# Optimization experiments

Hardware: AMD Instinct MI355X
Metric: run time of the kernel (lower is better)

The kernel has to match this reference:

```python
import jax, jax.numpy as jnp
import numpy as np

N_HEAD = 16
N_KV_HEADS = 4
N_REP = 4
HEAD_DIM = 128
N_EMBD = 2048
EPS = 1e-5
ROPE_BASE = 10000.0


def setup_inputs() -> dict:
    key = jax.random.key(0)
    ks = jax.random.split(key, 5)
    B, T, C = 2, 2048, N_EMBD
    s = 0.02
    return {
        "x": jax.random.normal(ks[0], (B, T, C), dtype=jnp.float32),
        "wq": jax.random.normal(ks[1], (C, N_HEAD * HEAD_DIM), dtype=jnp.float32) * s,
        "wk": jax.random.normal(ks[2], (C, N_KV_HEADS * HEAD_DIM), dtype=jnp.float32) * s,
        "wv": jax.random.normal(ks[3], (C, N_KV_HEADS * HEAD_DIM), dtype=jnp.float32) * s,
        "wc": jax.random.normal(ks[4], (C, C), dtype=jnp.float32) * s,
        "q_norm_w": jnp.ones((HEAD_DIM,), dtype=jnp.float32),
        "k_norm_w": jnp.ones((HEAD_DIM,), dtype=jnp.float32),
    }


def _rmsnorm(x, w):
    # norm in fp32, scale by weight (matches RMSNorm.forward)
    xf = x.astype(jnp.float32)
    rms = jax.lax.rsqrt(jnp.mean(xf * xf, axis=-1, keepdims=True) + EPS)
    return (xf * rms).astype(x.dtype) * w


def _rope(x, cos, sin):
    # x: [B,T,H,D]; cos/sin: [T, D//2]; interleaved even/odd rotation
    xf = x.astype(jnp.float32)
    xe = xf[..., 0::2]
    xo = xf[..., 1::2]
    c = cos[None, :, None, :]
    s = sin[None, :, None, :]
    ye = xe * c - xo * s
    yo = xe * s + xo * c
    y = jnp.stack((ye, yo), axis=-1).reshape(x.shape)
    return y.astype(x.dtype)


def reference(x, wq, wk, wv, wc, q_norm_w, k_norm_w):
    B, T, C = x.shape
    q = (x @ wq).reshape(B, T, N_HEAD, HEAD_DIM)
    k = (x @ wk).reshape(B, T, N_KV_HEADS, HEAD_DIM)
    v = (x @ wv).reshape(B, T, N_KV_HEADS, HEAD_DIM)

    q = _rmsnorm(q, q_norm_w)
    k = _rmsnorm(k, k_norm_w)

    inv_freq = 1.0 / (ROPE_BASE ** (jnp.arange(0, HEAD_DIM, 2, dtype=jnp.float32) / HEAD_DIM))
    theta = jnp.arange(T, dtype=jnp.float32)[:, None] * inv_freq[None, :]  # [T, D//2]
    cos, sin = jnp.cos(theta), jnp.sin(theta)
    q = _rope(q, cos, sin)
    k = _rope(k, cos, sin)

    # GQA: repeat kv heads (repeat_kv with n_rep)
    k = jnp.repeat(k, N_REP, axis=2)  # [B,T,H,D]
    v = jnp.repeat(v, N_REP, axis=2)

    scale = 1.0 / jnp.sqrt(jnp.float32(HEAD_DIM))
    scores = jnp.einsum("bthd,bshd->bhts", q, k) * scale  # [B,H,T,S]
    causal = jnp.tril(jnp.ones((T, T), dtype=bool))
    scores = jnp.where(causal[None, None], scores, jnp.finfo(scores.dtype).min)
    attn = jax.nn.softmax(scores, axis=-1)
    y = jnp.einsum("bhts,bshd->bthd", attn, v).reshape(B, T, C)
    return y @ wc
```

## Files before the change

kernel.cpp:

```cpp
#include <hip/hip_runtime.h>
#include <hip/hip_bf16.h>
#include <cstdint>
#include <cstddef>

using bf16 = __hip_bfloat16;
typedef __attribute__((ext_vector_type(8))) short short8;
typedef __attribute__((ext_vector_type(4))) float f32x4;
typedef __attribute__((ext_vector_type(16))) float f32x16;

#define T_SEQ 2048
#define NHEAD 16
#define NKV 4
#define HD 128
#define CE 2048

__device__ __forceinline__ void gl_lds16(const void* g, void* l) {
  __builtin_amdgcn_global_load_lds(
      (const __attribute__((address_space(1))) unsigned int*)g,
      (__attribute__((address_space(3))) unsigned int*)l, 16, 0, 0);
}

__device__ __forceinline__ unsigned int cvtpk_bf16(float lo, float hi) {
  unsigned int r;
  asm("v_cvt_pk_bf16_f32 %0, %1, %2" : "=v"(r) : "v"(lo), "v"(hi));
  return r;
}

__device__ __forceinline__ void plswap(unsigned int& x, unsigned int& y, int hi) {
#if __has_builtin(__builtin_amdgcn_permlane32_swap)
  auto r = __builtin_amdgcn_permlane32_swap(x, y, false, false);
  x = r[0];
  y = r[1];
#else
  unsigned int xp = (unsigned int)__shfl_xor((int)x, 32);
  unsigned int yp = (unsigned int)__shfl_xor((int)y, 32);
  unsigned int nx = hi ? yp : x;
  unsigned int ny = hi ? y : xp;
  x = nx;
  y = ny;
#endif
}

__global__ void __launch_bounds__(256) prep(const float* __restrict__ x,
                                            const float* __restrict__ wq,
                                            const float* __restrict__ wk,
                                            const float* __restrict__ wv,
                                            const float* __restrict__ wc,
                                            bf16* __restrict__ xb,
                                            bf16* __restrict__ wqkvt,
                                            bf16* __restrict__ wct) {
  __shared__ float tile[32][33];
  const int tid = threadIdx.x;
  int bb = blockIdx.x;
  if (bb < 8192) {
    const int i = bb * 256 + tid;
    const float4 v = ((const float4*)x)[i];
    bf16 b0 = __float2bfloat16(v.x), b1 = __float2bfloat16(v.y),
         b2 = __float2bfloat16(v.z), b3 = __float2bfloat16(v.w);
    ushort4 u;
    u.x = *(const unsigned short*)&b0; u.y = *(const unsigned short*)&b1;
    u.z = *(const unsigned short*)&b2; u.w = *(const unsigned short*)&b3;
    ((ushort4*)xb)[i] = u;
    return;
  }
  bb -= 8192;
  const float* W;
  bf16* Wt;
  int N, bx, by;
  if (bb < 4096) {
    W = wq; Wt = wqkvt; N = 2048; bx = bb & 63; by = bb >> 6;
  } else if (bb < 5120) {
    const int c = bb - 4096;
    W = wk; Wt = wqkvt + (size_t)2048 * 2048; N = 512; bx = c & 15; by = c >> 4;
  } else if (bb < 6144) {
    const int c = bb - 5120;
    W = wv; Wt = wqkvt + (size_t)2560 * 2048; N = 512; bx = c & 15; by = c >> 4;
  } else {
    const int c = bb - 6144;
    W = wc; Wt = wct; N = 2048; bx = c & 63; by = c >> 6;
  }
  const int tx = tid & 31, ty = tid >> 5;
#pragma unroll
  for (int i = 0; i < 4; i++) {
    const int r = by * 32 + ty + i * 8;
    tile[ty + i * 8][tx] = W[(size_t)r * N + bx * 32 + tx];
  }
  __syncthreads();
#pragma unroll
  for (int i = 0; i < 4; i++) {
    const int n = bx * 32 + ty + i * 8;
    Wt[(size_t)n * 2048 + by * 32 + tx] = __float2bfloat16(tile[tx][ty + i * 8]);
  }
}

template <int BM, int BN, int WM, int WN, bool OBF>
__global__ void __launch_bounds__(512, 2)
gemm8i(const bf16* __restrict__ A, const bf16* __restrict__ Bt,
       void* __restrict__ Cv, int M, int N, int K) {
  constexpr int AWS = BM / 2 / WM;
  constexpr int BWS = BN / 2 / WN;
  constexpr int MH = AWS / 16;
  constexpr int NH = BWS / 16;
  constexpr int AH = BM / 128;
  constexpr int BH = BN / 128;
  constexpr int G = 2 * AH + BH;
  __shared__ bf16 smA[2][BM * 64];
  __shared__ bf16 smB[2][BN * 64];

  const int tid = threadIdx.x, lane = tid & 63, wid = tid >> 6;
  const int l15 = lane & 15, l4 = lane >> 4;
  const int wr = wid / WN, wc = wid % WN;

  const int nwg = gridDim.x;
  const int q = nwg >> 3, r = nwg & 7;
  const int xcd = blockIdx.x & 7, lin = blockIdx.x >> 3;
  const int wg = (xcd < r ? xcd * (q + 1) : r * (q + 1) + (xcd - r) * q) + lin;
  const int gw = N / BN;
  const int by = wg / gw, bx = wg % gw;
  const int row0 = by * BM, col0 = bx * BN;
  const int NT = K >> 6;
  const int NI = NT >> 1;

  const bf16* Ag = A + (size_t)row0 * K;
  const bf16* Bg = Bt + (size_t)col0 * K;

  auto stA = [&](int t, int h, int pb) {
    const int k0 = t << 6;
#pragma unroll
    for (int j = 0; j < AH; j++) {
      const int c = (h * AH + j) * 512 + tid;
      const int rowi = c >> 3;
      gl_lds16(Ag + (size_t)rowi * K + k0 + (((c & 7) ^ (rowi & 7)) << 3),
               (void*)(&smA[pb][(size_t)c << 3]));
    }
  };
  auto stB = [&](int t, int h, int pb) {
    const int k0 = t << 6;
#pragma unroll
    for (int j = 0; j < BH; j++) {
      const int c = (h * BH + j) * 512 + tid;
      const int rowi = c >> 3;
      gl_lds16(Bg + (size_t)rowi * K + k0 + (((c & 7) ^ (rowi & 7)) << 3),
               (void*)(&smB[pb][(size_t)c << 3]));
    }
  };
  auto rdA = [&](const bf16* sA, int mh, short8 (&dst)[MH][2]) {
#pragma unroll
    for (int i = 0; i < MH; i++) {
      const int rowl = mh * (BM / 2) + wr * AWS + i * 16 + l15;
#pragma unroll
      for (int kk = 0; kk < 2; kk++)
        dst[i][kk] = *(const short8*)(sA + rowl * 64 +
                                      ((((kk << 2) | l4) ^ (rowl & 7)) << 3));
    }
  };
  auto rdB = [&](const bf16* sB, int nh, short8 (&dst)[NH][2]) {
#pragma unroll
    for (int j = 0; j < NH; j++) {
      const int rowl = nh * (BN / 2) + wc * BWS + j * 16 + l15;
#pragma unroll
      for (int kk = 0; kk < 2; kk++)
        dst[j][kk] = *(const short8*)(sB + rowl * 64 +
                                      ((((kk << 2) | l4) ^ (rowl & 7)) << 3));
    }
  };

  f32x4 acc[2][2][MH][NH];
#pragma unroll
  for (int mh = 0; mh < 2; mh++)
#pragma unroll
    for (int nh = 0; nh < 2; nh++)
#pragma unroll
      for (int i = 0; i < MH; i++)
#pragma unroll
        for (int j = 0; j < NH; j++) acc[mh][nh][i][j] = (f32x4){0.f, 0.f, 0.f, 0.f};

  auto mmq = [&](short8 (&a)[MH][2], short8 (&b)[NH][2], f32x4 (&ac)[MH][NH]) {
    __builtin_amdgcn_s_setprio(1);
#pragma unroll
    for (int i = 0; i < MH; i++)
#pragma unroll
      for (int j = 0; j < NH; j++)
#pragma unroll
        for (int kk = 0; kk < 2; kk++)
          ac[i][j] = __builtin_amdgcn_mfma_f32_16x16x32_bf16(a[i][kk], b[j][kk],
                                                             ac[i][j], 0, 0, 0);
    __builtin_amdgcn_s_setprio(0);
  };

  short8 a0[MH][2], a1[MH][2], b0[NH][2], b1[NH][2];

#define LGKM0_SB                                            \
  asm volatile("s_waitcnt lgkmcnt(0)" ::: "memory");        \
  __builtin_amdgcn_sched_barrier(0);
#define GATE_G                                              \
  asm volatile("s_waitcnt vmcnt(%0)" ::"i"(G) : "memory");

  stA(0, 0, 0); stB(0, 0, 0); stA(0, 1, 0); stB(0, 1, 0);
  stA(1, 0, 1); stB(1, 0, 1); stA(1, 1, 1);
  GATE_G
  __builtin_amdgcn_s_barrier();

  for (int i = 0; i < NI - 1; ++i) {
    const int u = 2 * i, v = u + 1;
    stB(v, 1, 1);
    rdA(smA[0], 0, a0); rdB(smB[0], 0, b0);
    __builtin_amdgcn_s_barrier();
    LGKM0_SB
    mmq(a0, b0, acc[0][0]);
    __builtin_amdgcn_s_barrier();
    stA(u + 2, 0, 0);
    rdA(smA[0], 1, a1);
    __builtin_amdgcn_s_barrier();
    LGKM0_SB
    mmq(a1, b0, acc[1][0]);
    __builtin_amdgcn_s_barrier();
    stB(u + 2, 0, 0);
    rdB(smB[0], 1, b1);
    __builtin_amdgcn_s_barrier();
    LGKM0_SB
    mmq(a1, b1, acc[1][1]);
    __builtin_amdgcn_s_barrier();
    stA(u + 2, 1, 0);
    mmq(a0, b1, acc[0][1]);
    GATE_G
    __builtin_amdgcn_s_barrier();
    stB(u + 2, 1, 0);
    rdA(smA[1], 0, a0); rdB(smB[1], 0, b0);
    __builtin_amdgcn_s_barrier();
    LGKM0_SB
    mmq(a0, b0, acc[0][0]);
    __builtin_amdgcn_s_barrier();
    stA(v + 2, 0, 1);
    rdA(smA[1], 1, a1);
    __builtin_amdgcn_s_barrier();
    LGKM0_SB
    mmq(a1, b0, acc[1][0]);
    __builtin_amdgcn_s_barrier();
    stB(v + 2, 0, 1);
    rdB(smB[1], 1, b1);
    __builtin_amdgcn_s_barrier();
    LGKM0_SB
    mmq(a1, b1, acc[1][1]);
    __builtin_amdgcn_s_barrier();
    stA(v + 2, 1, 1);
    mmq(a0, b1, acc[0][1]);
    GATE_G
    __builtin_amdgcn_s_barrier();
  }

  {
    stB(NT - 1, 1, 1);
    rdA(smA[0], 0, a0); rdB(smB[0], 0, b0);
    __builtin_amdgcn_s_barrier();
    LGKM0_SB
    mmq(a0, b0, acc[0][0]);
    __builtin_amdgcn_s_barrier();
    rdA(smA[0], 1, a1);
    __builtin_amdgcn_s_barrier();
    LGKM0_SB
    mmq(a1, b0, acc[1][0]);
    __builtin_amdgcn_s_barrier();
    rdB(smB[0], 1, b1);
    __builtin_amdgcn_s_barrier();
    LGKM0_SB
    mmq(a1, b1, acc[1][1]);
    __builtin_amdgcn_s_barrier();
    mmq(a0, b1, acc[0][1]);
    asm volatile("s_waitcnt vmcnt(0)" ::: "memory");
    __builtin_amdgcn_s_barrier();
    rdA(smA[1], 0, a0); rdB(smB[1], 0, b0);
    __builtin_amdgcn_s_barrier();
    LGKM0_SB
    mmq(a0, b0, acc[0][0]);
    __builtin_amdgcn_s_barrier();
    rdA(smA[1], 1, a1);
    __builtin_amdgcn_s_barrier();
    LGKM0_SB
    mmq(a1, b0, acc[1][0]);
    __builtin_amdgcn_s_barrier();
    rdB(smB[1], 1, b1);
    __builtin_amdgcn_s_barrier();
    LGKM0_SB
    mmq(a1, b1, acc[1][1]);
    mmq(a0, b1, acc[0][1]);
  }

#pragma unroll
  for (int mh = 0; mh < 2; mh++)
#pragma unroll
    for (int nh = 0; nh < 2; nh++)
#pragma unroll
      for (int i = 0; i < MH; i++)
#pragma unroll
        for (int j = 0; j < NH; j++)
#pragma unroll
          for (int rr = 0; rr < 4; rr++) {
            const size_t row = row0 + mh * (BM / 2) + wr * AWS + i * 16 + l4 * 4 + rr;
            const size_t col = col0 + nh * (BN / 2) + wc * BWS + j * 16 + l15;
            if constexpr (OBF)
              ((bf16*)Cv)[row * N + col] = __float2bfloat16(acc[mh][nh][i][j][rr]);
            else
              ((float*)Cv)[row * N + col] = acc[mh][nh][i][j][rr];
          }
#undef LGKM0_SB
#undef GATE_G
}

__global__ void __launch_bounds__(256) qkv_post(const bf16* __restrict__ QKV,
                                                const float* __restrict__ qw,
                                                const float* __restrict__ kw,
                                                bf16* __restrict__ Qo,
                                                bf16* __restrict__ Ko,
                                                bf16* __restrict__ Vto) {
  const int g = blockIdx.x * 4 + (threadIdx.x >> 6);
  const int lane = threadIdx.x & 63;
  const int hh = g % 24;
  const int bt = g / 24;
  const int b = bt >> 11, t = bt & (T_SEQ - 1);
  int off;
  if (hh < 16) off = hh * 128;
  else if (hh < 20) off = 2048 + (hh - 16) * 128;
  else off = 2560 + (hh - 20) * 128;
  const ushort2 xr = *(const ushort2*)(QKV + (size_t)bt * 3072 + off + lane * 2);
  const float xx = __bfloat162float(*(const bf16*)&xr.x);
  const float xy = __bfloat162float(*(const bf16*)&xr.y);
  if (hh < 20) {
    float ss = xx * xx + xy * xy;
    ss += __shfl_xor(ss, 1);  ss += __shfl_xor(ss, 2);  ss += __shfl_xor(ss, 4);
    ss += __shfl_xor(ss, 8);  ss += __shfl_xor(ss, 16); ss += __shfl_xor(ss, 32);
    const float rms = rsqrtf(ss * (1.0f / 128.0f) + 1e-5f);
    const float* w = (hh < 16) ? qw : kw;
    const float x0 = xx * rms * w[lane * 2];
    const float x1 = xy * rms * w[lane * 2 + 1];
    const float inv = exp2f((float)lane * (-13.287712379549449f / 64.0f));
    const float th = (float)t * inv;
    const float sn = sinf(th), cs = cosf(th);
    const float y0 = x0 * cs - x1 * sn;
    const float y1 = x0 * sn + x1 * cs;
    const bf16 o0 = __float2bfloat16(y0), o1 = __float2bfloat16(y1);
    if (hh < 16) {
      bf16* d = Qo + ((size_t)(b * NHEAD + hh) * T_SEQ + t) * HD + lane * 2;
      d[0] = o0; d[1] = o1;
    } else {
      bf16* d = Ko + ((size_t)(b * NKV + (hh - 16)) * T_SEQ + t) * HD + lane * 2;
      d[0] = o0; d[1] = o1;
    }
  } else {
    bf16* d = Vto + ((size_t)(b * NKV + (hh - 20)) * HD + lane * 2) * T_SEQ + t;
    d[0] = __float2bfloat16(xx);
    d[T_SEQ] = __float2bfloat16(xy);
  }
}

__global__ void __launch_bounds__(256, 2) attn_fwd(const bf16* __restrict__ Q,
                                                   const bf16* __restrict__ K,
                                                   const bf16* __restrict__ Vt,
                                                   bf16* __restrict__ Y) {
  __shared__ bf16 smK[128 * 128];
  __shared__ bf16 smV[128 * 128];

  const int bid = blockIdx.x;
  const int p = bid & 255, sdx = bid >> 8;
  const int bh = p & 31;
  const int jh = p >> 5;
  const int jq = sdx ? (15 - jh) : jh;
  const int h = bh & (NHEAD - 1), b = bh >> 4;
  const int bkv = b * NKV + (h >> 2);

  const int tid = threadIdx.x, wid = tid >> 6, lane = tid & 63;
  const int l31 = lane & 31, hi = lane >> 5;
  const int q0w = jq * 128 + wid * 32;

  const bf16* Kb = K + (size_t)bkv * T_SEQ * HD;
  const bf16* Vb = Vt + (size_t)bkv * HD * T_SEQ;

  const bf16* Qrow = Q + ((size_t)bh * T_SEQ + q0w + l31) * HD + hi * 8;
  short8 qf[8];
#pragma unroll
  for (int ds = 0; ds < 8; ds++) qf[ds] = *(const short8*)(Qrow + ds * 16);

  f32x16 o[4];
#pragma unroll
  for (int d = 0; d < 4; d++) o[d] = (f32x16)(0.f);
  float mrun = -INFINITY, lrun = 0.f;

  constexpr float CL = 0.08838834764831845f * 1.44269504088896340736f;
  const int trow = tid >> 4, tslot = tid & 15;

  const int ntiles = jq + 1;

  for (int t = 0; t < ntiles; t++) {
    const int k0 = t * 128;
    __syncthreads();
#pragma unroll
    for (int i = 0; i < 8; i++) {
      const int row = i * 16 + trow;
      const int ss = (tslot ^ (row & 15)) * 8;
      gl_lds16(Kb + (size_t)(k0 + row) * HD + ss, (void*)((char*)smK + i * 4096 + wid * 1024));
      gl_lds16(Vb + (size_t)row * T_SEQ + k0 + ss, (void*)((char*)smV + i * 4096 + wid * 1024));
    }
    __syncthreads();

    const bool lastt = (t == jq);
    const int glim = lastt ? wid : 3;

    f32x16 sg[4];
#pragma unroll
    for (int g = 0; g < 4; g++) {
      if (g > glim) continue;
      f32x16 acc = (f32x16)(0.f);
#pragma unroll
      for (int ds = 0; ds < 8; ds++) {
        const int row = g * 32 + l31;
        const short8 kf = *(const short8*)(smK + (size_t)row * 128 +
                                           (((ds << 1) | hi) ^ (row & 15)) * 8);
        acc = __builtin_amdgcn_mfma_f32_32x32x16_bf16(kf, qf[ds], acc, 0, 0, 0);
      }
      sg[g] = acc;
    }
    float tmax = -INFINITY;
#pragma unroll
    for (int g = 0; g < 4; g++) {
      if (g > glim) continue;
      if (lastt && g == wid) {
#pragma unroll
        for (int r = 0; r < 16; r++) {
          const int kr = (r & 3) + 8 * (r >> 2) + (hi << 2);
          if (kr > l31) sg[g][r] = -INFINITY;
        }
      }
#pragma unroll
      for (int r = 0; r < 16; r++) tmax = fmaxf(tmax, sg[g][r]);
    }
    tmax = fmaxf(tmax, __shfl_xor(tmax, 32));
    const float mnew = fmaxf(mrun, tmax);
    const float f = exp2f((mrun - mnew) * CL);
    mrun = mnew;
    lrun *= f;
#pragma unroll
    for (int d = 0; d < 4; d++)
#pragma unroll
      for (int r = 0; r < 16; r++) o[d][r] *= f;

    float lsum = 0.f;
#pragma unroll
    for (int g = 0; g < 4; g++) {
      if (g > glim) continue;
      float pp[16];
      float s0 = 0.f, s1 = 0.f;
#pragma unroll
      for (int r = 0; r < 16; r++) pp[r] = exp2f((sg[g][r] - mnew) * CL);
#pragma unroll
      for (int r = 0; r < 8; r++) { s0 += pp[2 * r]; s1 += pp[2 * r + 1]; }
      lsum += s0 + s1;

      unsigned int w0 = cvtpk_bf16(pp[0], pp[1]),  w2 = cvtpk_bf16(pp[4], pp[5]);
      unsigned int w1 = cvtpk_bf16(pp[2], pp[3]),  w3 = cvtpk_bf16(pp[6], pp[7]);
      unsigned int w4 = cvtpk_bf16(pp[8], pp[9]),  w6 = cvtpk_bf16(pp[12], pp[13]);
      unsigned int w5 = cvtpk_bf16(pp[10], pp[11]), w7 = cvtpk_bf16(pp[14], pp[15]);
      plswap(w0, w2, hi); plswap(w1, w3, hi);
      plswap(w4, w6, hi); plswap(w5, w7, hi);
      union { unsigned int u[4]; short8 s8; } pa0, pa1;
      pa0.u[0] = w0; pa0.u[1] = w1; pa0.u[2] = w2; pa0.u[3] = w3;
      pa1.u[0] = w4; pa1.u[1] = w5; pa1.u[2] = w6; pa1.u[3] = w7;

#pragma unroll
      for (int d = 0; d < 4; d++) {
        const int row = d * 32 + l31;
        const int ks0 = g * 2, ks1 = g * 2 + 1;
        const short8 vf0 = *(const short8*)(smV + (size_t)row * 128 +
                                            (((ks0 << 1) | hi) ^ (row & 15)) * 8);
        const short8 vf1 = *(const short8*)(smV + (size_t)row * 128 +
                                            (((ks1 << 1) | hi) ^ (row & 15)) * 8);
        o[d] = __builtin_amdgcn_mfma_f32_32x32x16_bf16(vf0, pa0.s8, o[d], 0, 0, 0);
        o[d] = __builtin_amdgcn_mfma_f32_32x32x16_bf16(vf1, pa1.s8, o[d], 0, 0, 0);
      }
    }
    lrun += lsum + __shfl_xor(lsum, 32);
  }

  const float inv = 1.0f / lrun;
  bf16* yrow = Y + ((size_t)(b * T_SEQ + q0w + l31)) * CE + h * HD;
#pragma unroll
  for (int d = 0; d < 4; d++) {
#pragma unroll
    for (int rg = 0; rg < 4; rg++) {
      ushort4 u;
      bf16 e0 = __float2bfloat16(o[d][rg * 4 + 0] * inv);
      bf16 e1 = __float2bfloat16(o[d][rg * 4 + 1] * inv);
      bf16 e2 = __float2bfloat16(o[d][rg * 4 + 2] * inv);
      bf16 e3 = __float2bfloat16(o[d][rg * 4 + 3] * inv);
      u.x = *(const unsigned short*)&e0; u.y = *(const unsigned short*)&e1;
      u.z = *(const unsigned short*)&e2; u.w = *(const unsigned short*)&e3;
      *(ushort4*)(yrow + d * 32 + rg * 8 + (hi << 2)) = u;
    }
  }
}

extern "C" void kernel_launch(void* const* d_in, const int* in_sizes, int n_in,
                              void* d_out, int out_size, void* d_ws, size_t ws_size,
                              hipStream_t stream) {
  const float* x   = (const float*)d_in[0];
  const float* wq  = (const float*)d_in[1];
  const float* wk  = (const float*)d_in[2];
  const float* wv  = (const float*)d_in[3];
  const float* wc  = (const float*)d_in[4];
  const float* qnw = (const float*)d_in[5];
  const float* knw = (const float*)d_in[6];
  float* out = (float*)d_out;

  char* ws = (char*)d_ws;
  bf16*  xb    = (bf16*)(ws);
  bf16*  wqkvt = (bf16*)(ws + 16777216);
  bf16*  wct   = (bf16*)(ws + 29360128);
  bf16*  qkv   = (bf16*)(ws + 37748736);
  bf16*  Qb    = (bf16*)(ws + 88080384);
  bf16*  Kb    = (bf16*)(ws + 104857600);
  bf16*  Vtb   = (bf16*)(ws + 109051904);
  bf16*  yb    = (bf16*)(ws + 113246208);

  prep<<<18432, 256, 0, stream>>>(x, wq, wk, wv, wc, xb, wqkvt, wct);
  gemm8i<256, 256, 2, 4, true><<<192, 512, 0, stream>>>(xb, wqkvt, qkv, 4096, 3072, 2048);
  qkv_post<<<24576, 256, 0, stream>>>(qkv, qnw, knw, Qb, Kb, Vtb);
  attn_fwd<<<512, 256, 0, stream>>>(Qb, Kb, Vtb, yb);
  gemm8i<128, 256, 2, 4, false><<<256, 512, 0, stream>>>(yb, wct, out, 4096, 2048, 2048);
}
```

Measured before the change: 221.1 us.

## Split long causal attention rows into KV partitions with a combine kernel

Replaces the paired query-tile scheduling with a job table that splits long causal query tiles into two or three KV-range partitions. Each partition writes unnormalized bf16 output plus running max and sum, and a new combine kernel merges them with log-sum-exp weights. This is meant to shorten the longest blocks and improve load balance across CUs. In exchange it adds extra global traffic, a second kernel launch, and some precision loss from storing the partials in bf16.

```diff
diff --git a/kernel.cpp b/kernel.cpp
--- a/kernel.cpp
+++ b/kernel.cpp
@@ -353,24 +353,42 @@
   }
 }
 
+__constant__ unsigned short JT[30] = {
+    0x0605, 0x160A, 0x160B, 0x266B, 0x160F,
+    0x0504, 0x1508, 0x1509, 0x2559, 0x256A, 0x150C, 0x150D, 0x255D,
+    0x150E, 0x255E, 0x35AE, 0x256F, 0x35BF,
+    0x0403, 0x1406, 0x1407, 0x2447, 0x2458, 0x245C, 0x349C, 0x34AD,
+    0x0302, 0x2346,
+    0x0201, 0x0100};
+
+#define ATTN_CL 0.12754125f
+
 __global__ void __launch_bounds__(256, 2) attn_fwd(const bf16* __restrict__ Q,
                                                    const bf16* __restrict__ K,
                                                    const bf16* __restrict__ Vt,
-                                                   bf16* __restrict__ Y) {
+                                                   bf16* __restrict__ Y,
+                                                   bf16* __restrict__ PO,
+                                                   float* __restrict__ PML) {
   __shared__ bf16 smK[128 * 128];
   __shared__ bf16 smV[128 * 128];
 
   const int bid = blockIdx.x;
-  const int p = bid & 255, sdx = bid >> 8;
-  const int bh = p & 31;
-  const int jh = p >> 5;
-  const int jq = sdx ? (15 - jh) : jh;
+  const int bh = bid & 31;
+  const int jobi = bid >> 5;
+  const unsigned int e = JT[jobi];
+  const int jq = e & 15;
+  const int lo = (e >> 4) & 15;
+  const int len = (e >> 8) & 15;
+  const int part = e >> 12;
+  const int hi_t = lo + len;
+
   const int h = bh & (NHEAD - 1), b = bh >> 4;
   const int bkv = b * NKV + (h >> 2);
 
   const int tid = threadIdx.x, wid = tid >> 6, lane = tid & 63;
   const int l31 = lane & 31, hi = lane >> 5;
   const int q0w = jq * 128 + wid * 32;
+  const int trow = tid >> 4, tslot = tid & 15;
 
   const bf16* Kb = K + (size_t)bkv * T_SEQ * HD;
   const bf16* Vb = Vt + (size_t)bkv * HD * T_SEQ;
@@ -385,12 +403,9 @@
   for (int d = 0; d < 4; d++) o[d] = (f32x16)(0.f);
   float mrun = -INFINITY, lrun = 0.f;
 
-  constexpr float CL = 0.08838834764831845f * 1.44269504088896340736f;
-  const int trow = tid >> 4, tslot = tid & 15;
-
-  const int ntiles = jq + 1;
-
-  for (int t = 0; t < ntiles; t++) {
+  constexpr float CL = ATTN_CL;
+
+  for (int t = lo; t < hi_t; t++) {
     const int k0 = t * 128;
     __syncthreads();
 #pragma unroll
@@ -402,8 +417,8 @@
     }
     __syncthreads();
 
-    const bool lastt = (t == jq);
-    const int glim = lastt ? wid : 3;
+    const bool diag = (t == jq);
+    const int glim = diag ? wid : 3;
 
     f32x16 sg[4];
 #pragma unroll
@@ -423,7 +438,7 @@
 #pragma unroll
     for (int g = 0; g < 4; g++) {
       if (g > glim) continue;
-      if (lastt && g == wid) {
+      if (diag && g == wid) {
 #pragma unroll
         for (int r = 0; r < 16; r++) {
           const int kr = (r & 3) + 8 * (r >> 2) + (hi << 2);
@@ -480,21 +495,118 @@
     lrun += lsum + __shfl_xor(lsum, 32);
   }
 
-  const float inv = 1.0f / lrun;
-  bf16* yrow = Y + ((size_t)(b * T_SEQ + q0w + l31)) * CE + h * HD;
-#pragma unroll
-  for (int d = 0; d < 4; d++) {
-#pragma unroll
-    for (int rg = 0; rg < 4; rg++) {
-      ushort4 u;
-      bf16 e0 = __float2bfloat16(o[d][rg * 4 + 0] * inv);
-      bf16 e1 = __float2bfloat16(o[d][rg * 4 + 1] * inv);
-      bf16 e2 = __float2bfloat16(o[d][rg * 4 + 2] * inv);
-      bf16 e3 = __float2bfloat16(o[d][rg * 4 + 3] * inv);
-      u.x = *(const unsigned short*)&e0; u.y = *(const unsigned short*)&e1;
-      u.z = *(const unsigned short*)&e2; u.w = *(const unsigned short*)&e3;
-      *(ushort4*)(yrow + d * 32 + rg * 8 + (hi << 2)) = u;
-    }
+  if (part == 0) {
+    const float inv = 1.0f / lrun;
+    bf16* yrow = Y + ((size_t)(b * T_SEQ + q0w + l31)) * CE + h * HD;
+#pragma unroll
+    for (int d = 0; d < 4; d++) {
+#pragma unroll
+      for (int rg = 0; rg < 4; rg++) {
+        ushort4 u;
+        bf16 e0 = __float2bfloat16(o[d][rg * 4 + 0] * inv);
+        bf16 e1 = __float2bfloat16(o[d][rg * 4 + 1] * inv);
+        bf16 e2 = __float2bfloat16(o[d][rg * 4 + 2] * inv);
+        bf16 e3 = __float2bfloat16(o[d][rg * 4 + 3] * inv);
+        u.x = *(const unsigned short*)&e0; u.y = *(const unsigned short*)&e1;
+        u.z = *(const unsigned short*)&e2; u.w = *(const unsigned short*)&e3;
+        *(ushort4*)(yrow + d * 32 + rg * 8 + (hi << 2)) = u;
+      }
+    }
+  } else {
+    const int plocal = (jq < 12) ? (jq - 6) * 2 + (part - 1)
+                                 : 12 + (jq - 12) * 3 + (part - 1);
+    const int pidx = bh * 24 + plocal;
+    bf16* po = PO + (size_t)pidx * 16384;
+    const int row = wid * 32 + l31;
+#pragma unroll
+    for (int d = 0; d < 4; d++) {
+#pragma unroll
+      for (int rg = 0; rg < 4; rg++) {
+        ushort4 u;
+        bf16 e0 = __float2bfloat16(o[d][rg * 4 + 0]);
+        bf16 e1 = __float2bfloat16(o[d][rg * 4 + 1]);
+        bf16 e2 = __float2bfloat16(o[d][rg * 4 + 2]);
+        bf16 e3 = __float2bfloat16(o[d][rg * 4 + 3]);
+        u.x = *(const unsigned short*)&e0; u.y = *(const unsigned short*)&e1;
+        u.z = *(const unsigned short*)&e2; u.w = *(const unsigned short*)&e3;
+        *(ushort4*)(po + (size_t)row * 128 + d * 32 + rg * 8 + (hi << 2)) = u;
+      }
+    }
+    if (hi == 0) {
+      PML[(size_t)pidx * 256 + row * 2 + 0] = mrun;
+      PML[(size_t)pidx * 256 + row * 2 + 1] = lrun;
+    }
+  }
+}
+
+__global__ void __launch_bounds__(256) attn_combine(const bf16* __restrict__ PO,
+                                                    const float* __restrict__ PML,
+                                                    bf16* __restrict__ Y) {
+  const int bid = blockIdx.x;
+  const int rb = bid & 3;
+  const int Jl = (bid >> 2) % 10;
+  const int bh = bid / 40;
+  const int J = 6 + Jl;
+  const bool has2 = (J >= 12);
+  const int base = bh * 24 + (has2 ? 12 + (J - 12) * 3 : (J - 6) * 2);
+  const int tid = threadIdx.x;
+  const int row = rb * 32 + (tid >> 3);
+  const int c0 = (tid & 7) * 16;
+  const int b = bh >> 4, h = bh & 15;
+
+  const float m0 = PML[(size_t)(base + 0) * 256 + row * 2 + 0];
+  const float l0 = PML[(size_t)(base + 0) * 256 + row * 2 + 1];
+  const float m1 = PML[(size_t)(base + 1) * 256 + row * 2 + 0];
+  const float l1 = PML[(size_t)(base + 1) * 256 + row * 2 + 1];
+  float m2 = -INFINITY, l2 = 0.f;
+  if (has2) {
+    m2 = PML[(size_t)(base + 2) * 256 + row * 2 + 0];
+    l2 = PML[(size_t)(base + 2) * 256 + row * 2 + 1];
+  }
+  const float mx = fmaxf(fmaxf(m0, m1), m2);
+  const float w0 = exp2f((m0 - mx) * ATTN_CL);
+  const float w1 = exp2f((m1 - mx) * ATTN_CL);
+  const float w2 = has2 ? exp2f((m2 - mx) * ATTN_CL) : 0.f;
+  const float inv = 1.0f / (w0 * l0 + w1 * l1 + w2 * l2);
+
+  const bf16* p0 = PO + (size_t)(base + 0) * 16384 + (size_t)row * 128 + c0;
+  const bf16* p1 = PO + (size_t)(base + 1) * 16384 + (size_t)row * 128 + c0;
+  const bf16* p2 = PO + (size_t)(base + 2) * 16384 + (size_t)row * 128 + c0;
+
+  float acc[16];
+#pragma unroll
+  for (int half = 0; half < 2; half++) {
+    const short8 v0 = *(const short8*)(p0 + half * 8);
+    const short8 v1 = *(const short8*)(p1 + half * 8);
+#pragma unroll
+    for (int i = 0; i < 8; i++) {
+      const unsigned short u0 = (unsigned short)v0[i], u1 = (unsigned short)v1[i];
+      acc[half * 8 + i] = w0 * __bfloat162float(*(const bf16*)&u0) +
+                          w1 * __bfloat162float(*(const bf16*)&u1);
+    }
+  }
+  if (has2) {
+#pragma unroll
+    for (int half = 0; half < 2; half++) {
+      const short8 v2 = *(const short8*)(p2 + half * 8);
+#pragma unroll
+      for (int i = 0; i < 8; i++) {
+        const unsigned short u2 = (unsigned short)v2[i];
+        acc[half * 8 + i] += w2 * __bfloat162float(*(const bf16*)&u2);
+      }
+    }
+  }
+
+  bf16* yp = Y + ((size_t)(b * T_SEQ + J * 128 + row)) * CE + h * HD + c0;
+#pragma unroll
+  for (int half = 0; half < 2; half++) {
+    short8 out;
+#pragma unroll
+    for (int i = 0; i < 8; i++) {
+      const bf16 ev = __float2bfloat16(acc[half * 8 + i] * inv);
+      out[i] = *(const short*)&ev;
+    }
+    *(short8*)(yp + half * 8) = out;
   }
 }
 
@@ -515,6 +627,8 @@
   bf16*  wqkvt = (bf16*)(ws + 16777216);
   bf16*  wct   = (bf16*)(ws + 29360128);
   bf16*  qkv   = (bf16*)(ws + 37748736);
+  bf16*  partO = (bf16*)(ws + 37748736);
+  float* partML= (float*)(ws + 62914560);
   bf16*  Qb    = (bf16*)(ws + 88080384);
   bf16*  Kb    = (bf16*)(ws + 104857600);
   bf16*  Vtb   = (bf16*)(ws + 109051904);
@@ -523,6 +637,7 @@
   prep<<<18432, 256, 0, stream>>>(x, wq, wk, wv, wc, xb, wqkvt, wct);
   gemm8i<256, 256, 2, 4, true><<<192, 512, 0, stream>>>(xb, wqkvt, qkv, 4096, 3072, 2048);
   qkv_post<<<24576, 256, 0, stream>>>(qkv, qnw, knw, Qb, Kb, Vtb);
-  attn_fwd<<<512, 256, 0, stream>>>(Qb, Kb, Vtb, yb);
+  attn_fwd<<<960, 256, 0, stream>>>(Qb, Kb, Vtb, yb, partO, partML);
+  attn_combine<<<1280, 256, 0, stream>>>(partO, partML, yb);
   gemm8i<128, 256, 2, 4, false><<<256, 512, 0, stream>>>(yb, wct, out, 4096, 2048, 2048);
 }
```

Result: no change. 218.0 us (median of 3 runs) (-1.4%).
